# Kernel tuning notes

Hardware: AMD Instinct MI355X
Metric: run time of the kernel (lower is better)

## Reference

```python
import jax, jax.numpy as jnp
import numpy as np

KS = 3          # kernel_size
P = (KS - 1) // 2  # padding size
OUT = 32        # output_features
B, C, H, W_DIM = 16, 3, 512, 512

def _kernel_coordinates():
    i, j = np.meshgrid(np.arange(KS), np.arange(KS))
    i = i.reshape(-1)
    j = j.reshape(-1)
    coords = np.dstack((i, j))[0]
    # drop the center (P, P), matching torch module
    return coords[np.any(coords != P, axis=1)]

COORDS = _kernel_coordinates()  # 8 offsets for KS=3


def setup_inputs() -> dict:
    key = jax.random.key(0)
    k1, k2, k3 = jax.random.split(key, 3)
    x = jax.random.normal(k1, (B, C, H, W_DIM), dtype=jnp.float32)
    W = jax.random.normal(k2, (OUT, C * len(COORDS)), dtype=jnp.float32) * 0.05
    b = jax.random.normal(k3, (OUT,), dtype=jnp.float32) * 0.05
    return {"x": x, "W": W, "b": b}


def reference(x, W, b):
    _, _, h, w = x.shape
    xp = jnp.pad(x, ((0, 0), (0, 0), (P, P), (P, P)))
    # shifted-neighbor minus center, concat over channel dim (order matches torch)
    chans = [xp[:, :, i:h + i, j:w + j] - x for i, j in COORDS]
    feat = jnp.concatenate(chans, axis=1)  # [B, 3*8, H, W]
    # 1x1 conv == channel contraction
    out = jnp.einsum('bchw,oc->bohw', feat, W) + b[None, :, None, None]
    return out
```

## Files before the change

kernel.cpp:

```cpp
#include <hip/hip_runtime.h>

#define HH 512
#define WW 512
#define CIN 3
#define COUT 32
#define NB 16

typedef float f4 __attribute__((ext_vector_type(4)));

__global__ __launch_bounds__(256)
void pointconv_kernel(const float* __restrict__ x,
                      const float* __restrict__ Wg,
                      const float* __restrict__ bias,
                      float* __restrict__ out) {
    __shared__ float Cb[COUT * 4];

    const int tid = threadIdx.y * 128 + threadIdx.x;
    if (tid < COUT) {
        const int o = tid;
        float cs0 = 0.f, cs1 = 0.f, cs2 = 0.f;
        #pragma unroll
        for (int k = 0; k < 8; ++k) {
            cs0 += Wg[o * 24 + k * 3 + 0];
            cs1 += Wg[o * 24 + k * 3 + 1];
            cs2 += Wg[o * 24 + k * 3 + 2];
        }
        Cb[o * 4 + 0] = -cs0;
        Cb[o * 4 + 1] = -cs1;
        Cb[o * 4 + 2] = -cs2;
        Cb[o * 4 + 3] = bias[o];
    }
    __syncthreads();

    const int b  = blockIdx.z;
    const int y  = blockIdx.y * 2 + threadIdx.y;
    const int x0 = threadIdx.x * 4;

    float v[3][3][6];
    #pragma unroll
    for (int c = 0; c < 3; ++c) {
        const float* xc = x + ((size_t)(b * CIN + c) * HH) * WW;
        #pragma unroll
        for (int r = 0; r < 3; ++r) {
            const int yy = y + r - 1;
            const bool rowok = (yy >= 0) && (yy < HH);
            const float* row = xc + (ptrdiff_t)yy * WW;
            f4 mid;
            if (rowok) {
                mid = *(const f4*)(row + x0);
            } else {
                mid = (f4){0.f, 0.f, 0.f, 0.f};
            }
            v[c][r][1] = mid.x; v[c][r][2] = mid.y;
            v[c][r][3] = mid.z; v[c][r][4] = mid.w;
            v[c][r][0] = (rowok && x0 > 0)        ? row[x0 - 1] : 0.f;
            v[c][r][5] = (rowok && x0 + 4 < WW)   ? row[x0 + 4] : 0.f;
        }
    }

    float* outp = out + (((size_t)b * COUT) * HH + y) * WW + x0;

    const int TI[8] = {0, 1, 2, 0, 2, 0, 1, 2};
    const int TJ[8] = {0, 0, 0, 1, 1, 2, 2, 2};

    #pragma unroll 2
    for (int o = 0; o < COUT; ++o) {
        const float* wo = Wg + o * 24;
        const f4 cb = *(const f4*)&Cb[o * 4];

        float a0 = cb.w, a1 = cb.w, a2 = cb.w, a3 = cb.w;
        #pragma unroll
        for (int k = 0; k < 8; ++k) {
            const int ty = TI[k], tx = TJ[k];
            #pragma unroll
            for (int c = 0; c < 3; ++c) {
                const float w = wo[k * 3 + c];
                a0 += w * v[c][ty][0 + tx];
                a1 += w * v[c][ty][1 + tx];
                a2 += w * v[c][ty][2 + tx];
                a3 += w * v[c][ty][3 + tx];
            }
        }
        a0 += cb.x * v[0][1][1]; a1 += cb.x * v[0][1][2];
        a2 += cb.x * v[0][1][3]; a3 += cb.x * v[0][1][4];
        a0 += cb.y * v[1][1][1]; a1 += cb.y * v[1][1][2];
        a2 += cb.y * v[1][1][3]; a3 += cb.y * v[1][1][4];
        a0 += cb.z * v[2][1][1]; a1 += cb.z * v[2][1][2];
        a2 += cb.z * v[2][1][3]; a3 += cb.z * v[2][1][4];

        f4 res = (f4){a0, a1, a2, a3};
        *(f4*)(outp + (size_t)o * (HH * WW)) = res;
    }
}

extern "C" void kernel_launch(void* const* d_in, const int* in_sizes, int n_in,
                              void* d_out, int out_size, void* d_ws, size_t ws_size,
                              hipStream_t stream) {
    const float* x    = (const float*)d_in[0];
    const float* Wg   = (const float*)d_in[1];
    const float* bias = (const float*)d_in[2];
    float* out = (float*)d_out;

    dim3 block(128, 2, 1);
    dim3 grid(1, 256, 16);
    hipLaunchKernelGGL(pointconv_kernel, grid, block, 0, stream, x, Wg, bias, out);
}
```

Baseline: 565.3 us.

## Assign one output channel per block and loop over row slabs

Each block now computes a single output channel over a 32-row slab, looping over row pairs, instead of all 32 channels for two rows. Weights become block-uniform scalars, removing the shared-memory setup and sync. Output writes per block become contiguous within one plane. The cost is re-reading the input tile once per output channel, increasing cache/memory read traffic.

```diff
diff --git a/kernel.cpp b/kernel.cpp
--- a/kernel.cpp
+++ b/kernel.cpp
@@ -13,62 +13,57 @@
                       const float* __restrict__ Wg,
                       const float* __restrict__ bias,
                       float* __restrict__ out) {
-    __shared__ float Cb[COUT * 4];
+    const int o    = blockIdx.x;
+    const int slab = blockIdx.y;
+    const int b    = blockIdx.z;
 
-    const int tid = threadIdx.y * 128 + threadIdx.x;
-    if (tid < COUT) {
-        const int o = tid;
-        float cs0 = 0.f, cs1 = 0.f, cs2 = 0.f;
-        #pragma unroll
-        for (int k = 0; k < 8; ++k) {
-            cs0 += Wg[o * 24 + k * 3 + 0];
-            cs1 += Wg[o * 24 + k * 3 + 1];
-            cs2 += Wg[o * 24 + k * 3 + 2];
-        }
-        Cb[o * 4 + 0] = -cs0;
-        Cb[o * 4 + 1] = -cs1;
-        Cb[o * 4 + 2] = -cs2;
-        Cb[o * 4 + 3] = bias[o];
+    const float* wo = Wg + o * 24;
+    float cneg0 = 0.f, cneg1 = 0.f, cneg2 = 0.f;
+    #pragma unroll
+    for (int k = 0; k < 8; ++k) {
+        cneg0 -= wo[k * 3 + 0];
+        cneg1 -= wo[k * 3 + 1];
+        cneg2 -= wo[k * 3 + 2];
     }
-    __syncthreads();
+    const float bv = bias[o];
 
-    const int b  = blockIdx.z;
-    const int y  = blockIdx.y * 2 + threadIdx.y;
-    const int x0 = threadIdx.x * 4;
-
-    float v[3][3][6];
-    #pragma unroll
-    for (int c = 0; c < 3; ++c) {
-        const float* xc = x + ((size_t)(b * CIN + c) * HH) * WW;
-        #pragma unroll
-        for (int r = 0; r < 3; ++r) {
-            const int yy = y + r - 1;
-            const bool rowok = (yy >= 0) && (yy < HH);
-            const float* row = xc + (ptrdiff_t)yy * WW;
-            f4 mid;
-            if (rowok) {
-                mid = *(const f4*)(row + x0);
-            } else {
-                mid = (f4){0.f, 0.f, 0.f, 0.f};
-            }
-            v[c][r][1] = mid.x; v[c][r][2] = mid.y;
-            v[c][r][3] = mid.z; v[c][r][4] = mid.w;
-            v[c][r][0] = (rowok && x0 > 0)        ? row[x0 - 1] : 0.f;
-            v[c][r][5] = (rowok && x0 + 4 < WW)   ? row[x0 + 4] : 0.f;
-        }
-    }
-
-    float* outp = out + (((size_t)b * COUT) * HH + y) * WW + x0;
+    const int tid  = threadIdx.x;
+    const int rsub = tid >> 7;
+    const int col  = (tid & 127) * 4;
 
     const int TI[8] = {0, 1, 2, 0, 2, 0, 1, 2};
     const int TJ[8] = {0, 0, 0, 1, 1, 2, 2, 2};
 
-    #pragma unroll 2
-    for (int o = 0; o < COUT; ++o) {
-        const float* wo = Wg + o * 24;
-        const f4 cb = *(const f4*)&Cb[o * 4];
+    const float* xb   = x + (size_t)b * CIN * HH * WW;
+    float*       outp = out + (((size_t)b * COUT + o) * HH) * WW;
 
-        float a0 = cb.w, a1 = cb.w, a2 = cb.w, a3 = cb.w;
+    #pragma unroll 1
+    for (int p = 0; p < 16; ++p) {
+        const int y = slab * 32 + p * 2 + rsub;
+
+        float v[3][3][6];
+        #pragma unroll
+        for (int c = 0; c < 3; ++c) {
+            const float* xc = xb + (size_t)c * HH * WW;
+            #pragma unroll
+            for (int r = 0; r < 3; ++r) {
+                const int yy = y + r - 1;
+                const bool rowok = (yy >= 0) && (yy < HH);
+                const float* row = xc + (ptrdiff_t)yy * WW;
+                f4 mid;
+                if (rowok) {
+                    mid = *(const f4*)(row + col);
+                } else {
+                    mid = (f4){0.f, 0.f, 0.f, 0.f};
+                }
+                v[c][r][1] = mid.x; v[c][r][2] = mid.y;
+                v[c][r][3] = mid.z; v[c][r][4] = mid.w;
+                v[c][r][0] = (rowok && col > 0)        ? row[col - 1] : 0.f;
+                v[c][r][5] = (rowok && col + 4 < WW)   ? row[col + 4] : 0.f;
+            }
+        }
+
+        float a0 = bv, a1 = bv, a2 = bv, a3 = bv;
         #pragma unroll
         for (int k = 0; k < 8; ++k) {
             const int ty = TI[k], tx = TJ[k];
@@ -81,15 +76,14 @@
                 a3 += w * v[c][ty][3 + tx];
             }
         }
-        a0 += cb.x * v[0][1][1]; a1 += cb.x * v[0][1][2];
-        a2 += cb.x * v[0][1][3]; a3 += cb.x * v[0][1][4];
-        a0 += cb.y * v[1][1][1]; a1 += cb.y * v[1][1][2];
-        a2 += cb.y * v[1][1][3]; a3 += cb.y * v[1][1][4];
-        a0 += cb.z * v[2][1][1]; a1 += cb.z * v[2][1][2];
-        a2 += cb.z * v[2][1][3]; a3 += cb.z * v[2][1][4];
+        a0 += cneg0 * v[0][1][1]; a1 += cneg0 * v[0][1][2];
+        a2 += cneg0 * v[0][1][3]; a3 += cneg0 * v[0][1][4];
+        a0 += cneg1 * v[1][1][1]; a1 += cneg1 * v[1][1][2];
+        a2 += cneg1 * v[1][1][3]; a3 += cneg1 * v[1][1][4];
+        a0 += cneg2 * v[2][1][1]; a1 += cneg2 * v[2][1][2];
+        a2 += cneg2 * v[2][1][3]; a3 += cneg2 * v[2][1][4];
 
-        f4 res = (f4){a0, a1, a2, a3};
-        *(f4*)(outp + (size_t)o * (HH * WW)) = res;
+        *(f4*)(outp + (size_t)y * WW + col) = (f4){a0, a1, a2, a3};
     }
 }
 
@@ -101,7 +95,7 @@
     const float* bias = (const float*)d_in[2];
     float* out = (float*)d_out;
 
-    dim3 block(128, 2, 1);
-    dim3 grid(1, 256, 16);
+    dim3 block(256, 1, 1);
+    dim3 grid(32, 16, 16);
     hipLaunchKernelGGL(pointconv_kernel, grid, block, 0, stream, x, Wg, bias, out);
 }
```

Result: slower. 1.193 ms (+111.0%).
